# Kernel optimization log

Measured on AMD Instinct MI355X. Metric: run time of the kernel, lower is better.

The kernel has to match this reference:

```python
import jax, jax.numpy as jnp
import numpy as np

N, E, IN_DIM, HID, LAT, G = 100000, 1600000, 64, 128, 64, 1000
BN_EPS = 1e-5
LN_EPS = 1e-5


def _bn(x, g, b, m, v):
    # BatchNorm1d in eval mode: running stats
    return (x - m) * jax.lax.rsqrt(v + BN_EPS) * g + b


def setup_inputs() -> dict:
    key = jax.random.key(0)
    ks = iter(jax.random.split(key, 64))
    d = {}
    d["x"] = jax.random.normal(next(ks), (N, IN_DIM), jnp.float32)
    d["edge_index"] = jax.random.randint(next(ks), (2, E), 0, N, jnp.int32)
    d["batch"] = jnp.sort(jax.random.randint(next(ks), (N,), 0, G, jnp.int32))

    def lin(k, i, o):
        k1, k2 = jax.random.split(k)
        s = 1.0 / np.sqrt(i)
        return (jax.random.uniform(k1, (i, o), jnp.float32, -s, s),
                jax.random.uniform(k2, (o,), jnp.float32, -s, s))

    def bn_params(k, dim):
        g = 1.0 + 0.1 * jax.random.normal(k, (dim,), jnp.float32)
        return g, jnp.zeros(dim), jnp.zeros(dim), jnp.ones(dim)

    # input BN
    d["in_g"], d["in_b"], d["in_m"], d["in_v"] = bn_params(next(ks), IN_DIM)
    # conv layer 0 (in_dim -> hid)
    d["eps0"] = jnp.zeros(())
    d["c0_w1"], d["c0_b1"] = lin(next(ks), IN_DIM, HID)
    d["c0_g"], d["c0_bb"], d["c0_m"], d["c0_v"] = bn_params(next(ks), HID)
    d["c0_w2"], d["c0_b2"] = lin(next(ks), HID, HID)
    d["bn0_g"], d["bn0_b"], d["bn0_m"], d["bn0_v"] = bn_params(next(ks), HID)
    # conv layers 1..2 stacked (hid -> hid)
    def stack(fn):
        a = [fn(next(ks)) for _ in range(2)]
        return tuple(jnp.stack([t[i] for t in a]) for i in range(len(a[0])))
    d["epsR"] = jnp.zeros((2,))
    d["cR_w1"], d["cR_b1"] = stack(lambda k: lin(k, HID, HID))
    d["cR_g"], d["cR_bb"], d["cR_m"], d["cR_v"] = stack(lambda k: bn_params(k, HID))
    d["cR_w2"], d["cR_b2"] = stack(lambda k: lin(k, HID, HID))
    d["bnR_g"], d["bnR_b"], d["bnR_m"], d["bnR_v"] = stack(lambda k: bn_params(k, HID))
    # head
    d["fc1_w"], d["fc1_b"] = lin(next(ks), HID, HID)
    d["ln_g"] = jnp.ones(HID); d["ln_b"] = jnp.zeros(HID)
    d["fc2_w"], d["fc2_b"] = lin(next(ks), HID, LAT)
    return d


def _gin_layer(x, src, dst, eps, w1, b1, g, bb, m, v, w2, b2, og, ob, om, ov):
    # GINConv with sum aggregation: (1+eps)*x + scatter_sum(x[src] -> dst)
    agg = jax.ops.segment_sum(x[src], dst, num_segments=N)
    h = (1.0 + eps) * x + agg
    # GatedResidualMLP: Linear -> BN -> GELU -> (dropout off) -> Linear
    h = _bn(h @ w1 + b1, g, bb, m, v)
    h = jax.nn.gelu(h, approximate=False)
    h = h @ w2 + b2
    # outer BN -> GELU
    return jax.nn.gelu(_bn(h, og, ob, om, ov), approximate=False)


def reference(x, edge_index, batch, in_g, in_b, in_m, in_v,
              eps0, c0_w1, c0_b1, c0_g, c0_bb, c0_m, c0_v, c0_w2, c0_b2,
              bn0_g, bn0_b, bn0_m, bn0_v,
              epsR, cR_w1, cR_b1, cR_g, cR_bb, cR_m, cR_v, cR_w2, cR_b2,
              bnR_g, bnR_b, bnR_m, bnR_v,
              fc1_w, fc1_b, ln_g, ln_b, fc2_w, fc2_b):
    src, dst = edge_index[0], edge_index[1]
    h = _bn(x, in_g, in_b, in_m, in_v)
    h = _gin_layer(h, src, dst, eps0, c0_w1, c0_b1, c0_g, c0_bb, c0_m, c0_v,
                   c0_w2, c0_b2, bn0_g, bn0_b, bn0_m, bn0_v)
    for l in range(2):
        h = _gin_layer(h, src, dst, epsR[l], cR_w1[l], cR_b1[l], cR_g[l],
                       cR_bb[l], cR_m[l], cR_v[l], cR_w2[l], cR_b2[l],
                       bnR_g[l], bnR_b[l], bnR_m[l], bnR_v[l])
    # global mean pool over graphs
    sums = jax.ops.segment_sum(h, batch, num_segments=G)
    cnt = jax.ops.segment_sum(jnp.ones((N,), h.dtype), batch, num_segments=G)
    pooled = sums / jnp.maximum(cnt, 1.0)[:, None]
    # head: fc1 -> LayerNorm -> GELU -> residual -> fc2
    o = pooled @ fc1_w + fc1_b
    mu = jnp.mean(o, -1, keepdims=True)
    var = jnp.var(o, -1, keepdims=True)
    o = (o - mu) * jax.lax.rsqrt(var + LN_EPS) * ln_g + ln_b
    o = jax.nn.gelu(o, approximate=False) + pooled
    return o @ fc2_w + fc2_b
```

## Files before the change

### kernel.cpp

```cpp
#include <hip/hip_runtime.h>

#define BN_EPS 1e-5f
#define LN_EPS 1e-5f

typedef unsigned int uint;
typedef unsigned short ushort;
typedef __bf16 bf16_t;
typedef bf16_t bf16x8 __attribute__((ext_vector_type(8)));
typedef float f32x4 __attribute__((ext_vector_type(4)));

__device__ __forceinline__ float gelu_f(float x){
    return 0.5f * x * (1.0f + erff(x * 0.7071067811865475f));
}
__device__ __forceinline__ ushort f2bf(float f){
    union { float f; uint u; } x; x.f = f;
    uint r = (x.u + 0x7FFF + ((x.u >> 16) & 1)) >> 16;
    return (ushort)r;
}
__device__ __forceinline__ float bf2f(ushort u){
    union { uint u; float f; } x; x.u = ((uint)u) << 16;
    return x.f;
}

__global__ void zero_i32(int* __restrict__ p, int n){
    int i = blockIdx.x*blockDim.x + threadIdx.x;
    if (i < n) p[i] = 0;
}
__global__ void zero_f32(float* __restrict__ p, int n){
    int i = blockIdx.x*blockDim.x + threadIdx.x;
    if (i < n) p[i] = 0.0f;
}

__global__ void bn_input(const float* __restrict__ x,
                         const float* __restrict__ g, const float* __restrict__ b,
                         const float* __restrict__ m, const float* __restrict__ v,
                         ushort* __restrict__ out, int n4){
    int i = blockIdx.x*blockDim.x + threadIdx.x;
    if (i >= n4) return;
    int c0 = (i & 15) * 4;
    float4 xv = ((const float4*)x)[i];
    ushort o[4];
    #pragma unroll
    for (int j = 0; j < 4; j++){
        int c = c0 + j;
        float s  = g[c] * rsqrtf(v[c] + BN_EPS);
        float sh = b[c] - m[c]*s;
        o[j] = f2bf((&xv.x)[j]*s + sh);
    }
    uint2 pk = make_uint2((uint)o[0] | ((uint)o[1]<<16), (uint)o[2] | ((uint)o[3]<<16));
    ((uint2*)out)[i] = pk;
}

__global__ void pack_w(const float* __restrict__ w, ushort* __restrict__ out, int K){
    int t = blockIdx.x*blockDim.x + threadIdx.x;
    int total = (K/32)*8*64;
    if (t >= total) return;
    int lane = t & 63;
    int rem = t >> 6;
    int nf = rem & 7;
    int kk = rem >> 3;
    int kg = lane >> 4;
    int col = nf*16 + (lane & 15);
    uint r[4];
    #pragma unroll
    for (int p = 0; p < 4; p++){
        int k0 = kk*32 + kg*8 + p*2;
        ushort lo = f2bf(w[(size_t)k0*128 + col]);
        ushort hi = f2bf(w[(size_t)(k0+1)*128 + col]);
        r[p] = (uint)lo | ((uint)hi << 16);
    }
    *(uint4*)(out + (size_t)t*8) = make_uint4(r[0], r[1], r[2], r[3]);
}


__global__ __launch_bounds__(256) void bucket_count(const int* __restrict__ dst,
        int* __restrict__ bcnt, int E, int NB){
    __shared__ int h[1024];
    int tid = threadIdx.x;
    for (int i = tid; i < 1024; i += 256) h[i] = 0;
    __syncthreads();
    for (long i = (long)blockIdx.x*blockDim.x + tid; i < E; i += (long)gridDim.x*blockDim.x)
        atomicAdd(&h[dst[i] >> 8], 1);
    __syncthreads();
    for (int i = tid; i < NB; i += 256)
        if (h[i]) atomicAdd(&bcnt[i], h[i]);
}

__global__ __launch_bounds__(1024) void bucket_scan(const int* __restrict__ bcnt,
        int* __restrict__ boff, int* __restrict__ bcur, int NB, int E){
    __shared__ int s[1024];
    int tid = threadIdx.x;
    int v = (tid < NB) ? bcnt[tid] : 0;
    s[tid] = v; __syncthreads();
    for (int off = 1; off < 1024; off <<= 1){
        int t = s[tid];
        if (tid >= off) t += s[tid-off];
        __syncthreads(); s[tid] = t; __syncthreads();
    }
    if (tid < NB){ int ex = s[tid] - v; boff[tid] = ex; bcur[tid] = ex; }
    if (tid == 0) boff[NB] = E;
}

#define PCH 16384
__global__ __launch_bounds__(512) void partition_kernel(const int* __restrict__ src,
        const int* __restrict__ dst, int* __restrict__ bcur,
        uint* __restrict__ pairs, int E, int NB){
    __shared__ ushort rnk[PCH];
    __shared__ int cnt[1024];
    __shared__ int base[1024];
    int tid = threadIdx.x;
    long chunk0 = (long)blockIdx.x * PCH;
    for (int i = tid; i < 1024; i += 512) cnt[i] = 0;
    __syncthreads();
    for (int k = 0; k < PCH/512; k++){
        int el = k*512 + tid;
        long i = chunk0 + el;
        if (i < E){
            int b = dst[i] >> 8;
            rnk[el] = (ushort)atomicAdd(&cnt[b], 1);
        }
    }
    __syncthreads();
    for (int b = tid; b < NB; b += 512)
        if (cnt[b] > 0) base[b] = atomicAdd(&bcur[b], cnt[b]);
    __syncthreads();
    for (int k = 0; k < PCH/512; k++){
        int el = k*512 + tid;
        long i = chunk0 + el;
        if (i < E){
            int d = dst[i];
            int b = d >> 8;
            int pos = base[b] + (int)rnk[el];
            pairs[pos] = ((uint)(d & 255) << 24) | (uint)src[i];
        }
    }
}

#define BCAP 12288
__global__ __launch_bounds__(256) void bucket_build(const uint* __restrict__ pairs,
        const int* __restrict__ boff, int* __restrict__ rowptr,
        int* __restrict__ csrc, int N, int E, int NB){
    __shared__ int deg[256];
    __shared__ int scn[256];
    __shared__ int cur[256];
    __shared__ uint outl[BCAP];
    int b = blockIdx.x, tid = threadIdx.x;
    int e0 = boff[b], e1 = boff[b+1];
    int M = e1 - e0;
    deg[tid] = 0;
    __syncthreads();
    for (int e = tid; e < M; e += 256){
        uint p = pairs[e0 + e];
        atomicAdd(&deg[p >> 24], 1);
    }
    __syncthreads();
    int v = deg[tid];
    scn[tid] = v; __syncthreads();
    for (int off = 1; off < 256; off <<= 1){
        int t = scn[tid];
        if (tid >= off) t += scn[tid-off];
        __syncthreads(); scn[tid] = t; __syncthreads();
    }
    int excl = scn[tid] - v;
    int node = b*256 + tid;
    if (node < N) rowptr[node] = e0 + excl;
    if (b == NB-1 && tid == 0) rowptr[N] = E;
    cur[tid] = excl;
    __syncthreads();
    if (M <= BCAP){
        for (int e = tid; e < M; e += 256){
            uint p = pairs[e0 + e];
            int lp = atomicAdd(&cur[p >> 24], 1);
            outl[lp] = p & 0xFFFFFFu >> 8 ? (p & 0x00FFFFFFu) : (p & 0x00FFFFFFu);
        }
        __syncthreads();
        for (int e = tid; e < M; e += 256)
            csrc[e0 + e] = (int)(outl[e]);
    } else {
        for (int e = tid; e < M; e += 256){
            uint p = pairs[e0 + e];
            int lp = atomicAdd(&cur[p >> 24], 1);
            csrc[e0 + lp] = (int)(p & 0x00FFFFFFu);
        }
    }
}

__global__ __launch_bounds__(256) void agg_d64(const ushort* __restrict__ hin,
        const int* __restrict__ rowptr, const int* __restrict__ csrc,
        const float* __restrict__ epsp, int epsidx,
        ushort* __restrict__ hout, int n){
    int w = blockIdx.x*4 + (threadIdx.x >> 6);
    if (w >= n) return;
    int lane = threadIdx.x & 63;
    float eps1 = 1.0f + epsp[epsidx];
    int beg = rowptr[w], end = rowptr[w+1];
    float acc = 0.0f;
    if (end > beg){
        int last = end - 1;
        for (int j = beg; j < end; j += 8){
            int s[8];
            #pragma unroll
            for (int u = 0; u < 8; u++){
                int jj = j + u;
                s[u] = csrc[jj < last ? jj : last];
            }
            ushort t[8];
            #pragma unroll
            for (int u = 0; u < 8; u++) t[u] = hin[(size_t)s[u]*64 + lane];
            #pragma unroll
            for (int u = 0; u < 8; u++){
                float vv = bf2f(t[u]);
                acc += ((j + u) < end) ? vv : 0.f;
            }
        }
    }
    float self = bf2f(hin[(size_t)w*64 + lane]);
    hout[(size_t)w*64 + lane] = f2bf(eps1*self + acc);
}

__global__ __launch_bounds__(256) void agg_d128(const ushort* __restrict__ hin,
        const int* __restrict__ rowptr, const int* __restrict__ csrc,
        const float* __restrict__ epsp, int epsidx,
        ushort* __restrict__ hout, int n){
    int w = blockIdx.x*4 + (threadIdx.x >> 6);
    if (w >= n) return;
    int lane = threadIdx.x & 63;
    float eps1 = 1.0f + epsp[epsidx];
    int beg = rowptr[w], end = rowptr[w+1];
    const uint* h2 = (const uint*)hin;
    float ax = 0.f, ay = 0.f;
    if (end > beg){
        int last = end - 1;
        for (int j = beg; j < end; j += 8){
            int s[8];
            #pragma unroll
            for (int u = 0; u < 8; u++){
                int jj = j + u;
                s[u] = csrc[jj < last ? jj : last];
            }
            uint t[8];
            #pragma unroll
            for (int u = 0; u < 8; u++) t[u] = h2[(size_t)s[u]*64 + lane];
            #pragma unroll
            for (int u = 0; u < 8; u++){
                bool ok = (j + u) < end;
                float vx = bf2f((ushort)(t[u] & 0xFFFF));
                float vy = bf2f((ushort)(t[u] >> 16));
                ax += ok ? vx : 0.f;
                ay += ok ? vy : 0.f;
            }
        }
    }
    uint c = h2[(size_t)w*64 + lane];
    float ox = eps1*bf2f((ushort)(c & 0xFFFF)) + ax;
    float oy = eps1*bf2f((ushort)(c >> 16)) + ay;
    ((uint*)hout)[(size_t)w*64 + lane] = (uint)f2bf(ox) | ((uint)f2bf(oy) << 16);
}

template<int DIN>
__global__ __launch_bounds__(256) void mlp_mfma(
        const ushort* __restrict__ hin,
        const ushort* __restrict__ w1p, const float* __restrict__ b1,
        const float* __restrict__ g1, const float* __restrict__ bb1,
        const float* __restrict__ m1, const float* __restrict__ v1,
        const ushort* __restrict__ w2p, const float* __restrict__ b2,
        const float* __restrict__ g2, const float* __restrict__ bb2,
        const float* __restrict__ m2, const float* __restrict__ v2,
        ushort* __restrict__ hout, int n)
{
    constexpr int K1 = DIN/32;
    __shared__ ushort lds[64*128];
    __shared__ float mulA[128], addA[128], mulB[128], addB[128];
    int tid = threadIdx.x;
    int lane = tid & 63;
    int wv = tid >> 6;
    int row0 = blockIdx.x * 64;

    if (tid < 128){
        float s1 = g1[tid]*rsqrtf(v1[tid]+BN_EPS);
        mulA[tid] = s1; addA[tid] = (b1[tid]-m1[tid])*s1 + bb1[tid];
        float s2 = g2[tid]*rsqrtf(v2[tid]+BN_EPS);
        mulB[tid] = s2; addB[tid] = (b2[tid]-m2[tid])*s2 + bb2[tid];
    }

    constexpr int CPR = DIN/8;
    for (int idx = tid; idx < 64*CPR; idx += 256){
        int r = idx / CPR, c = idx - r*CPR;
        uint4 val = make_uint4(0,0,0,0);
        if (row0 + r < n) val = *(const uint4*)(hin + (size_t)(row0+r)*DIN + c*8);
        int byte = (r*DIN + c*8)*2;
        byte ^= (r & 7) << 4;
        *(uint4*)((char*)lds + byte) = val;
    }
    __syncthreads();

    int r16 = lane & 15;
    int kg = lane >> 4;
    int arow = wv*16 + r16;

    f32x4 acc[8];
    #pragma unroll
    for (int nf = 0; nf < 8; nf++) acc[nf] = (f32x4){0.f,0.f,0.f,0.f};
    #pragma unroll
    for (int kk = 0; kk < K1; kk++){
        int abyte = (arow*DIN + kk*32 + kg*8)*2;
        abyte ^= (arow & 7) << 4;
        bf16x8 af = *(const bf16x8*)((const char*)lds + abyte);
        #pragma unroll
        for (int nf = 0; nf < 8; nf++){
            bf16x8 bfr = *(const bf16x8*)(w1p + ((size_t)((kk*8 + nf)*64 + lane))*8);
            acc[nf] = __builtin_amdgcn_mfma_f32_16x16x32_bf16(af, bfr, acc[nf], 0, 0, 0);
        }
    }
    __syncthreads();

    #pragma unroll
    for (int nf = 0; nf < 8; nf++){
        int col = nf*16 + r16;
        float mu = mulA[col], ad = addA[col];
        #pragma unroll
        for (int r = 0; r < 4; r++){
            int row = wv*16 + kg*4 + r;
            float xg = gelu_f(acc[nf][r]*mu + ad);
            int byte = (row*128 + col)*2;
            byte ^= (row & 7) << 4;
            *(ushort*)((char*)lds + byte) = f2bf(xg);
        }
    }
    __syncthreads();

    f32x4 acc2[8];
    #pragma unroll
    for (int nf = 0; nf < 8; nf++) acc2[nf] = (f32x4){0.f,0.f,0.f,0.f};
    #pragma unroll
    for (int kk = 0; kk < 4; kk++){
        int abyte = (arow*128 + kk*32 + kg*8)*2;
        abyte ^= (arow & 7) << 4;
        bf16x8 af = *(const bf16x8*)((const char*)lds + abyte);
        #pragma unroll
        for (int nf = 0; nf < 8; nf++){
            bf16x8 bfr = *(const bf16x8*)(w2p + ((size_t)((kk*8 + nf)*64 + lane))*8);
            acc2[nf] = __builtin_amdgcn_mfma_f32_16x16x32_bf16(af, bfr, acc2[nf], 0, 0, 0);
        }
    }
    __syncthreads();

    #pragma unroll
    for (int nf = 0; nf < 8; nf++){
        int col = nf*16 + r16;
        float mu = mulB[col], ad = addB[col];
        #pragma unroll
        for (int r = 0; r < 4; r++){
            int row = wv*16 + kg*4 + r;
            float xg = gelu_f(acc2[nf][r]*mu + ad);
            int byte = (row*128 + col)*2;
            byte ^= (row & 7) << 4;
            *(ushort*)((char*)lds + byte) = f2bf(xg);
        }
    }
    __syncthreads();

    for (int idx = tid; idx < 64*16; idx += 256){
        int r = idx >> 4, c = idx & 15;
        if (row0 + r < n){
            int byte = (r*128 + c*8)*2;
            byte ^= (r & 7) << 4;
            uint4 v = *(const uint4*)((const char*)lds + byte);
            *(uint4*)(hout + (size_t)(row0+r)*128 + c*8) = v;
        }
    }
}

__global__ __launch_bounds__(128) void pool_kernel(const ushort* __restrict__ h,
        const int* __restrict__ batch, float* __restrict__ pool,
        float* __restrict__ cnt, int n){
    int c = threadIdx.x;
    int n0 = blockIdx.x * 32;
    float run = 0.f;
    float runc = 0.f;
    int curg = -1;
    for (int t = 0; t < 32; ++t){
        int node = n0 + t;
        if (node >= n) break;
        int gph = batch[node];
        if (gph != curg){
            if (curg >= 0){
                atomicAdd(&pool[curg*128 + c], run);
                if (c == 0) atomicAdd(&cnt[curg], runc);
            }
            curg = gph; run = 0.f; runc = 0.f;
        }
        run += bf2f(h[(size_t)node*128 + c]);
        runc += 1.f;
    }
    if (curg >= 0){
        atomicAdd(&pool[curg*128 + c], run);
        if (c == 0) atomicAdd(&cnt[curg], runc);
    }
}

__global__ __launch_bounds__(128) void head_kernel(const float* __restrict__ pool,
        const float* __restrict__ cnt,
        const float* __restrict__ fc1w, const float* __restrict__ fc1b,
        const float* __restrict__ lng, const float* __restrict__ lnb,
        const float* __restrict__ fc2w, const float* __restrict__ fc2b,
        float* __restrict__ out, int G){
    __shared__ float p[128];
    __shared__ float q[128];
    __shared__ float red[128];
    int g = blockIdx.x, c = threadIdx.x;
    float inv = 1.0f / fmaxf(cnt[g], 1.0f);
    float pv = pool[g*128 + c] * inv;
    p[c] = pv;
    __syncthreads();
    float o = fc1b[c];
    for (int k = 0; k < 128; k++) o = fmaf(p[k], fc1w[k*128 + c], o);
    red[c] = o; __syncthreads();
    for (int s = 64; s > 0; s >>= 1){ if (c < s) red[c] += red[c+s]; __syncthreads(); }
    float mu = red[0] * (1.0f/128.0f);
    __syncthreads();
    float d = o - mu;
    red[c] = d*d; __syncthreads();
    for (int s = 64; s > 0; s >>= 1){ if (c < s) red[c] += red[c+s]; __syncthreads(); }
    float var = red[0] * (1.0f/128.0f);
    __syncthreads();
    float xn = d * rsqrtf(var + LN_EPS) * lng[c] + lnb[c];
    float qv = gelu_f(xn) + pv;
    q[c] = qv;
    __syncthreads();
    if (c < 64){
        float a = fc2b[c];
        for (int k = 0; k < 128; k++) a = fmaf(q[k], fc2w[k*64 + c], a);
        out[g*64 + c] = a;
    }
}

extern "C" void kernel_launch(void* const* d_in, const int* in_sizes, int n_in,
                              void* d_out, int out_size, void* d_ws, size_t ws_size,
                              hipStream_t stream){
    const float* x     = (const float*)d_in[0];
    const int*   ei    = (const int*)d_in[1];
    const int*   batch = (const int*)d_in[2];
    const float* in_g  = (const float*)d_in[3];
    const float* in_b  = (const float*)d_in[4];
    const float* in_m  = (const float*)d_in[5];
    const float* in_v  = (const float*)d_in[6];
    const float* eps0  = (const float*)d_in[7];
    const float* c0_w1 = (const float*)d_in[8];
    const float* c0_b1 = (const float*)d_in[9];
    const float* c0_g  = (const float*)d_in[10];
    const float* c0_bb = (const float*)d_in[11];
    const float* c0_m  = (const float*)d_in[12];
    const float* c0_v  = (const float*)d_in[13];
    const float* c0_w2 = (const float*)d_in[14];
    const float* c0_b2 = (const float*)d_in[15];
    const float* bn0_g = (const float*)d_in[16];
    const float* bn0_b = (const float*)d_in[17];
    const float* bn0_m = (const float*)d_in[18];
    const float* bn0_v = (const float*)d_in[19];
    const float* epsR  = (const float*)d_in[20];
    const float* cR_w1 = (const float*)d_in[21];
    const float* cR_b1 = (const float*)d_in[22];
    const float* cR_g  = (const float*)d_in[23];
    const float* cR_bb = (const float*)d_in[24];
    const float* cR_m  = (const float*)d_in[25];
    const float* cR_v  = (const float*)d_in[26];
    const float* cR_w2 = (const float*)d_in[27];
    const float* cR_b2 = (const float*)d_in[28];
    const float* bnR_g = (const float*)d_in[29];
    const float* bnR_b = (const float*)d_in[30];
    const float* bnR_m = (const float*)d_in[31];
    const float* bnR_v = (const float*)d_in[32];
    const float* fc1_w = (const float*)d_in[33];
    const float* fc1_b = (const float*)d_in[34];
    const float* ln_g  = (const float*)d_in[35];
    const float* ln_b  = (const float*)d_in[36];
    const float* fc2_w = (const float*)d_in[37];
    const float* fc2_b = (const float*)d_in[38];

    const int N = in_sizes[0] / 64;
    const int E = in_sizes[1] / 2;
    const int G = out_size / 64;
    const int NB = (N + 255) >> 8;
    const int* srcp = ei;
    const int* dstp = ei + E;

    char* ws = (char*)d_ws;
    size_t off = 0;
    auto alloc = [&](size_t bytes)->char*{
        char* p = ws + off;
        off = (off + bytes + 255) & ~(size_t)255;
        return p;
    };
    ushort* bufA   = (ushort*)alloc((size_t)N*128*2);
    ushort* bufB   = (ushort*)alloc((size_t)N*128*2);
    int*    rowptr = (int*)   alloc((size_t)(N+1)*4);
    int*    csrc   = (int*)   alloc((size_t)E*4);
    uint*   pairs  = (uint*)  alloc((size_t)E*4);
    int*    bcnt   = (int*)   alloc((size_t)1025*4);
    int*    boff   = (int*)   alloc((size_t)1025*4);
    int*    bcur   = (int*)   alloc((size_t)1024*4);
    float*  pool   = (float*) alloc((size_t)G*128*4);
    float*  cnt    = (float*) alloc((size_t)G*4);
    ushort* pw0_1  = (ushort*)alloc((size_t)64*128*2);
    ushort* pw0_2  = (ushort*)alloc((size_t)128*128*2);
    ushort* pwR_1  = (ushort*)alloc((size_t)2*128*128*2);
    ushort* pwR_2  = (ushort*)alloc((size_t)2*128*128*2);
    (void)ws_size; (void)n_in;

    pack_w<<<(1024 + 255)/256, 256, 0, stream>>>(c0_w1, pw0_1, 64);
    pack_w<<<(2048 + 255)/256, 256, 0, stream>>>(c0_w2, pw0_2, 128);
    for (int l = 0; l < 2; l++){
        pack_w<<<(2048 + 255)/256, 256, 0, stream>>>(cR_w1 + (size_t)l*128*128, pwR_1 + (size_t)l*128*128, 128);
        pack_w<<<(2048 + 255)/256, 256, 0, stream>>>(cR_w2 + (size_t)l*128*128, pwR_2 + (size_t)l*128*128, 128);
    }

    zero_i32<<<(NB + 255)/256, 256, 0, stream>>>(bcnt, NB);
    bucket_count<<<1024, 256, 0, stream>>>(dstp, bcnt, E, NB);
    bucket_scan<<<1, 1024, 0, stream>>>(bcnt, boff, bcur, NB, E);
    partition_kernel<<<(E + PCH-1)/PCH, 512, 0, stream>>>(srcp, dstp, bcur, pairs, E, NB);
    bucket_build<<<NB, 256, 0, stream>>>(pairs, boff, rowptr, csrc, N, E, NB);

    bn_input<<<(N*16 + 255)/256, 256, 0, stream>>>(x, in_g, in_b, in_m, in_v, bufA, N*16);

    const int agg_blocks = (N + 3)/4;
    const int mlp_blocks = (N + 63)/64;

    agg_d64<<<agg_blocks, 256, 0, stream>>>(bufA, rowptr, csrc, eps0, 0, bufB, N);
    mlp_mfma<64><<<mlp_blocks, 256, 0, stream>>>(bufB,
        pw0_1, c0_b1, c0_g, c0_bb, c0_m, c0_v,
        pw0_2, c0_b2, bn0_g, bn0_b, bn0_m, bn0_v, bufA, N);

    for (int l = 0; l < 2; l++){
        agg_d128<<<agg_blocks, 256, 0, stream>>>(bufA, rowptr, csrc, epsR, l, bufB, N);
        mlp_mfma<128><<<mlp_blocks, 256, 0, stream>>>(bufB,
            pwR_1 + (size_t)l*128*128, cR_b1 + l*128, cR_g + l*128, cR_bb + l*128,
            cR_m + l*128, cR_v + l*128,
            pwR_2 + (size_t)l*128*128, cR_b2 + l*128, bnR_g + l*128, bnR_b + l*128,
            bnR_m + l*128, bnR_v + l*128, bufA, N);
    }

    zero_f32<<<(G*128 + 255)/256, 256, 0, stream>>>(pool, G*128);
    zero_f32<<<(G + 255)/256, 256, 0, stream>>>(cnt, G);
    pool_kernel<<<(N + 31)/32, 128, 0, stream>>>(bufA, batch, pool, cnt, N);
    head_kernel<<<G, 128, 0, stream>>>(pool, cnt, fc1_w, fc1_b, ln_g, ln_b,
                                       fc2_w, fc2_b, (float*)d_out, G);
}
```

Before: 446.0 us.

## Double MLP row tile per block, prefetch weights, use tanh-form GELU

The MLP kernel now handles 128 rows per block, with each wave computing two 16-row MFMA tiles that share every weight fragment load. The first K-slice of the weights is prefetched before the LDS fill. Block-wide barriers are dropped where each wave touches only its own rows. The erf-based GELU in the node MLPs is replaced by a tanh-form approximation built on exp2 and reciprocal intrinsics, which trades exactness for cheaper math; the head keeps the exact GELU. More LDS and registers per block may lower occupancy.

```diff
diff --git a/kernel.cpp b/kernel.cpp
--- a/kernel.cpp
+++ b/kernel.cpp
@@ -9,8 +9,14 @@
 typedef bf16_t bf16x8 __attribute__((ext_vector_type(8)));
 typedef float f32x4 __attribute__((ext_vector_type(4)));
 
-__device__ __forceinline__ float gelu_f(float x){
+__device__ __forceinline__ float gelu_exact(float x){
     return 0.5f * x * (1.0f + erff(x * 0.7071067811865475f));
+}
+__device__ __forceinline__ float gelu_fast(float x){
+    float z = x*(0.79788456f + 0.03567740814f*(x*x));
+    z = fminf(fmaxf(z, -15.f), 15.f);
+    float t = __builtin_amdgcn_exp2f(2.885390082f*z);
+    return x*t*__builtin_amdgcn_rcpf(t + 1.0f);
 }
 __device__ __forceinline__ ushort f2bf(float f){
     union { float f; uint u; } x; x.f = f;
@@ -171,7 +177,7 @@
         for (int e = tid; e < M; e += 256){
             uint p = pairs[e0 + e];
             int lp = atomicAdd(&cur[p >> 24], 1);
-            outl[lp] = p & 0xFFFFFFu >> 8 ? (p & 0x00FFFFFFu) : (p & 0x00FFFFFFu);
+            outl[lp] = p & 0x00FFFFFFu;
         }
         __syncthreads();
         for (int e = tid; e < M; e += 256)
@@ -269,12 +275,12 @@
         ushort* __restrict__ hout, int n)
 {
     constexpr int K1 = DIN/32;
-    __shared__ ushort lds[64*128];
+    __shared__ ushort lds[128*128];
     __shared__ float mulA[128], addA[128], mulB[128], addB[128];
     int tid = threadIdx.x;
     int lane = tid & 63;
     int wv = tid >> 6;
-    int row0 = blockIdx.x * 64;
+    int row0 = blockIdx.x * 128;
 
     if (tid < 128){
         float s1 = g1[tid]*rsqrtf(v1[tid]+BN_EPS);
@@ -283,88 +289,107 @@
         mulB[tid] = s2; addB[tid] = (b2[tid]-m2[tid])*s2 + bb2[tid];
     }
 
+    bf16x8 wpre[8];
+    #pragma unroll
+    for (int nf = 0; nf < 8; nf++)
+        wpre[nf] = *(const bf16x8*)(w1p + ((size_t)(nf*64 + lane))*8);
+
     constexpr int CPR = DIN/8;
-    for (int idx = tid; idx < 64*CPR; idx += 256){
+    for (int idx = tid; idx < 128*CPR; idx += 256){
         int r = idx / CPR, c = idx - r*CPR;
         uint4 val = make_uint4(0,0,0,0);
         if (row0 + r < n) val = *(const uint4*)(hin + (size_t)(row0+r)*DIN + c*8);
-        int byte = (r*DIN + c*8)*2;
-        byte ^= (r & 7) << 4;
+        int byte = (r*DIN + c*8)*2 ^ ((r & 7) << 4);
         *(uint4*)((char*)lds + byte) = val;
     }
     __syncthreads();
 
     int r16 = lane & 15;
     int kg = lane >> 4;
-    int arow = wv*16 + r16;
-
-    f32x4 acc[8];
-    #pragma unroll
-    for (int nf = 0; nf < 8; nf++) acc[nf] = (f32x4){0.f,0.f,0.f,0.f};
+    int arow = wv*32 + r16;
+
+    f32x4 acc[2][8];
+    #pragma unroll
+    for (int m = 0; m < 2; m++)
+        #pragma unroll
+        for (int nf = 0; nf < 8; nf++) acc[m][nf] = (f32x4){0.f,0.f,0.f,0.f};
     #pragma unroll
     for (int kk = 0; kk < K1; kk++){
-        int abyte = (arow*DIN + kk*32 + kg*8)*2;
-        abyte ^= (arow & 7) << 4;
-        bf16x8 af = *(const bf16x8*)((const char*)lds + abyte);
+        int ab0 = (arow*DIN + kk*32 + kg*8)*2 ^ ((arow & 7) << 4);
+        bf16x8 a0 = *(const bf16x8*)((const char*)lds + ab0);
+        bf16x8 a1 = *(const bf16x8*)((const char*)lds + ab0 + DIN*32);
         #pragma unroll
         for (int nf = 0; nf < 8; nf++){
-            bf16x8 bfr = *(const bf16x8*)(w1p + ((size_t)((kk*8 + nf)*64 + lane))*8);
-            acc[nf] = __builtin_amdgcn_mfma_f32_16x16x32_bf16(af, bfr, acc[nf], 0, 0, 0);
-        }
-    }
-    __syncthreads();
-
-    #pragma unroll
-    for (int nf = 0; nf < 8; nf++){
-        int col = nf*16 + r16;
-        float mu = mulA[col], ad = addA[col];
-        #pragma unroll
-        for (int r = 0; r < 4; r++){
-            int row = wv*16 + kg*4 + r;
-            float xg = gelu_f(acc[nf][r]*mu + ad);
-            int byte = (row*128 + col)*2;
-            byte ^= (row & 7) << 4;
-            *(ushort*)((char*)lds + byte) = f2bf(xg);
-        }
-    }
-    __syncthreads();
-
-    f32x4 acc2[8];
-    #pragma unroll
-    for (int nf = 0; nf < 8; nf++) acc2[nf] = (f32x4){0.f,0.f,0.f,0.f};
-    #pragma unroll
-    for (int kk = 0; kk < 4; kk++){
-        int abyte = (arow*128 + kk*32 + kg*8)*2;
-        abyte ^= (arow & 7) << 4;
-        bf16x8 af = *(const bf16x8*)((const char*)lds + abyte);
+            bf16x8 w = (kk == 0) ? wpre[nf]
+                     : *(const bf16x8*)(w1p + ((size_t)((kk*8 + nf)*64 + lane))*8);
+            acc[0][nf] = __builtin_amdgcn_mfma_f32_16x16x32_bf16(a0, w, acc[0][nf], 0, 0, 0);
+            acc[1][nf] = __builtin_amdgcn_mfma_f32_16x16x32_bf16(a1, w, acc[1][nf], 0, 0, 0);
+        }
+    }
+
+    if constexpr (DIN == 64) __syncthreads();
+
+    bf16x8 wpre2[8];
+    #pragma unroll
+    for (int nf = 0; nf < 8; nf++)
+        wpre2[nf] = *(const bf16x8*)(w2p + ((size_t)(nf*64 + lane))*8);
+
+    #pragma unroll
+    for (int m = 0; m < 2; m++){
         #pragma unroll
         for (int nf = 0; nf < 8; nf++){
-            bf16x8 bfr = *(const bf16x8*)(w2p + ((size_t)((kk*8 + nf)*64 + lane))*8);
-            acc2[nf] = __builtin_amdgcn_mfma_f32_16x16x32_bf16(af, bfr, acc2[nf], 0, 0, 0);
-        }
-    }
-    __syncthreads();
-
-    #pragma unroll
-    for (int nf = 0; nf < 8; nf++){
-        int col = nf*16 + r16;
-        float mu = mulB[col], ad = addB[col];
+            int col = nf*16 + r16;
+            float mu = mulA[col], ad = addA[col];
+            #pragma unroll
+            for (int r = 0; r < 4; r++){
+                int row = wv*32 + m*16 + kg*4 + r;
+                float xg = gelu_fast(acc[m][nf][r]*mu + ad);
+                int byte = (row*128 + col)*2 ^ ((row & 7) << 4);
+                *(ushort*)((char*)lds + byte) = f2bf(xg);
+            }
+        }
+    }
+
+    f32x4 acc2[2][8];
+    #pragma unroll
+    for (int m = 0; m < 2; m++)
         #pragma unroll
-        for (int r = 0; r < 4; r++){
-            int row = wv*16 + kg*4 + r;
-            float xg = gelu_f(acc2[nf][r]*mu + ad);
-            int byte = (row*128 + col)*2;
-            byte ^= (row & 7) << 4;
-            *(ushort*)((char*)lds + byte) = f2bf(xg);
-        }
-    }
-    __syncthreads();
-
-    for (int idx = tid; idx < 64*16; idx += 256){
+        for (int nf = 0; nf < 8; nf++) acc2[m][nf] = (f32x4){0.f,0.f,0.f,0.f};
+    #pragma unroll
+    for (int kk = 0; kk < 4; kk++){
+        int ab0 = (arow*128 + kk*32 + kg*8)*2 ^ ((arow & 7) << 4);
+        bf16x8 a0 = *(const bf16x8*)((const char*)lds + ab0);
+        bf16x8 a1 = *(const bf16x8*)((const char*)lds + ab0 + 128*32);
+        #pragma unroll
+        for (int nf = 0; nf < 8; nf++){
+            bf16x8 w = (kk == 0) ? wpre2[nf]
+                     : *(const bf16x8*)(w2p + ((size_t)((kk*8 + nf)*64 + lane))*8);
+            acc2[0][nf] = __builtin_amdgcn_mfma_f32_16x16x32_bf16(a0, w, acc2[0][nf], 0, 0, 0);
+            acc2[1][nf] = __builtin_amdgcn_mfma_f32_16x16x32_bf16(a1, w, acc2[1][nf], 0, 0, 0);
+        }
+    }
+
+    #pragma unroll
+    for (int m = 0; m < 2; m++){
+        #pragma unroll
+        for (int nf = 0; nf < 8; nf++){
+            int col = nf*16 + r16;
+            float mu = mulB[col], ad = addB[col];
+            #pragma unroll
+            for (int r = 0; r < 4; r++){
+                int row = wv*32 + m*16 + kg*4 + r;
+                float xg = gelu_fast(acc2[m][nf][r]*mu + ad);
+                int byte = (row*128 + col)*2 ^ ((row & 7) << 4);
+                *(ushort*)((char*)lds + byte) = f2bf(xg);
+            }
+        }
+    }
+    __syncthreads();
+
+    for (int idx = tid; idx < 128*16; idx += 256){
         int r = idx >> 4, c = idx & 15;
         if (row0 + r < n){
-            int byte = (r*128 + c*8)*2;
-            byte ^= (r & 7) << 4;
+            int byte = (r*128 + c*8)*2 ^ ((r & 7) << 4);
             uint4 v = *(const uint4*)((const char*)lds + byte);
             *(uint4*)(hout + (size_t)(row0+r)*128 + c*8) = v;
         }
@@ -425,7 +450,7 @@
     float var = red[0] * (1.0f/128.0f);
     __syncthreads();
     float xn = d * rsqrtf(var + LN_EPS) * lng[c] + lnb[c];
-    float qv = gelu_f(xn) + pv;
+    float qv = gelu_exact(xn) + pv;
     q[c] = qv;
     __syncthreads();
     if (c < 64){
@@ -524,7 +549,7 @@
     bn_input<<<(N*16 + 255)/256, 256, 0, stream>>>(x, in_g, in_b, in_m, in_v, bufA, N*16);
 
     const int agg_blocks = (N + 3)/4;
-    const int mlp_blocks = (N + 63)/64;
+    const int mlp_blocks = (N + 127)/128;
 
     agg_d64<<<agg_blocks, 256, 0, stream>>>(bufA, rowptr, csrc, eps0, 0, bufB, N);
     mlp_mfma<64><<<mlp_blocks, 256, 0, stream>>>(bufB,
```

Result: faster. 384.1 us (-13.9%).
